# Kernel optimization log

Hardware: AMD Instinct MI355X
Metric: run time of the kernel (lower is better)

The kernel has to match this reference:

```python
import jax, jax.numpy as jnp
import numpy as np

BATCH, SEQ, D_IN, D_OUT = 32, 1024, 128, 128
NEG_SLOPE = 0.1


def setup_inputs() -> dict:
    key = jax.random.key(0)
    k1, k2, k3, k4 = jax.random.split(key, 4)
    nodes = jax.random.normal(k1, (BATCH, SEQ, D_IN), dtype=jnp.float32)
    adjacent = jax.random.randint(k2, (BATCH, SEQ, SEQ), 0, 2, dtype=jnp.int32)
    W = jax.random.normal(k3, (D_IN, D_OUT), dtype=jnp.float32) / np.sqrt(D_IN)
    B = jax.random.normal(k4, (D_IN, D_OUT), dtype=jnp.float32) / np.sqrt(D_IN)
    return {"nodes": nodes, "adjacent": adjacent, "W": W, "B": B}


def reference(nodes, adjacent, W, B):
    # mask[b, out, in] = 1 if edge (out -> in) present
    mask = (adjacent != 0).astype(nodes.dtype)
    # counts[b, in] = in-degree (number of 'out' neighbors pooled per target node)
    counts = mask.sum(axis=1)                               # [b, s_in]
    # segment-sum of neighbor features: pooled[b, in, d] = sum_out mask * nodes[b, out, d]
    pooled = jnp.einsum('boi,bod->bid', mask, nodes)        # [b, s_in, d]
    # mean over neighbors; nodes with zero degree get no pooled contribution
    pooled = jnp.where(counts[..., None] > 0,
                       pooled / jnp.maximum(counts, 1.0)[..., None],
                       jnp.zeros((), dtype=nodes.dtype))
    updated = nodes @ B + pooled @ W                        # [b, s, d_out]
    return jax.nn.leaky_relu(updated, negative_slope=NEG_SLOPE)
```

## Files before the change

kernel.cpp:

```cpp
#include <hip/hip_runtime.h>
#include <hip/hip_bf16.h>

#define SEQ 1024
#define DIM 128
#define NEG_SLOPE 0.1f

typedef __bf16 bf16x8 __attribute__((ext_vector_type(8)));
typedef float f32x4v __attribute__((ext_vector_type(4)));
typedef unsigned short ushort8 __attribute__((ext_vector_type(8)));

__global__ __launch_bounds__(256, 2)
void gcn_fused(const float* __restrict__ nodes,
               const int* __restrict__ adj,
               const float* __restrict__ W,
               const float* __restrict__ Bm,
               float* __restrict__ out)
{
    __shared__ float inv_lds[64];
    __shared__ __bf16 pooled_lds[64][136];

    const int bid   = blockIdx.x;
    const int xcd   = bid & 7;
    const int slot  = bid >> 3;
    const int batch = ((slot >> 4) << 3) | xcd;
    const int mtile = slot & 15;
    const int i0    = mtile << 6;

    const int tid  = threadIdx.x;
    const int wave = tid >> 6;
    const int lane = tid & 63;
    const int wm   = wave >> 1;
    const int wn   = wave & 1;
    const int lrow = lane & 15;
    const int quad = lane >> 4;

    const int*   __restrict__ adj_b   = adj   + (size_t)batch * SEQ * SEQ;
    const float* __restrict__ nodes_b = nodes + (size_t)batch * SEQ * DIM;

    f32x4v acc[2][4] = {};
    int cnt0 = 0, cnt1 = 0;

    const int i_a0 = i0 + wm * 32 + lrow;
    const int d_b0 = wn * 64 + lrow;

    const int*   pa = adj_b   + (size_t)(quad * 8) * SEQ + i_a0;
    const float* pb = nodes_b + (size_t)(quad * 8) * DIM + d_b0;

    #pragma unroll 2
    for (int ks = 0; ks < 32; ++ks) {
        ushort8 au0, au1;
        bf16x8  bv[4];
        #pragma unroll
        for (int j = 0; j < 8; ++j) {
            const int x0 = pa[(size_t)j * SEQ];
            const int x1 = pa[(size_t)j * SEQ + 16];
            cnt0 += (x0 != 0);
            cnt1 += (x1 != 0);
            au0[j] = (x0 != 0) ? (unsigned short)0x3F80 : (unsigned short)0;
            au1[j] = (x1 != 0) ? (unsigned short)0x3F80 : (unsigned short)0;
        }
        #pragma unroll
        for (int nf = 0; nf < 4; ++nf) {
            #pragma unroll
            for (int j = 0; j < 8; ++j)
                bv[nf][j] = (__bf16)pb[j * DIM + nf * 16];
        }
        const bf16x8 av0 = __builtin_bit_cast(bf16x8, au0);
        const bf16x8 av1 = __builtin_bit_cast(bf16x8, au1);
        #pragma unroll
        for (int nf = 0; nf < 4; ++nf)
            acc[0][nf] = __builtin_amdgcn_mfma_f32_16x16x32_bf16(av0, bv[nf], acc[0][nf], 0, 0, 0);
        #pragma unroll
        for (int nf = 0; nf < 4; ++nf)
            acc[1][nf] = __builtin_amdgcn_mfma_f32_16x16x32_bf16(av1, bv[nf], acc[1][nf], 0, 0, 0);
        pa += 32 * SEQ;
        pb += 32 * DIM;
    }

    {
        int c0 = cnt0;
        c0 += __shfl_xor(c0, 16);
        c0 += __shfl_xor(c0, 32);
        int c1 = cnt1;
        c1 += __shfl_xor(c1, 16);
        c1 += __shfl_xor(c1, 32);
        if (wn == 0 && quad == 0) {
            inv_lds[wm * 32 + lrow]      = (c0 > 0) ? 1.0f / (float)c0 : 0.0f;
            inv_lds[wm * 32 + 16 + lrow] = (c1 > 0) ? 1.0f / (float)c1 : 0.0f;
        }
    }
    __syncthreads();

    #pragma unroll
    for (int mf = 0; mf < 2; ++mf) {
        #pragma unroll
        for (int r = 0; r < 4; ++r) {
            const int row = wm * 32 + mf * 16 + quad * 4 + r;
            const float inv = inv_lds[row];
            #pragma unroll
            for (int nf = 0; nf < 4; ++nf) {
                const int col = wn * 64 + nf * 16 + lrow;
                pooled_lds[row][col] = (__bf16)(acc[mf][nf][r] * inv);
            }
        }
    }
    __syncthreads();

    f32x4v acc2[2][4] = {};

    #pragma unroll
    for (int ks = 0; ks < 4; ++ks) {
        const int k0 = ks * 32 + quad * 8;
        bf16x8 av[2];
        #pragma unroll
        for (int mf = 0; mf < 2; ++mf)
            av[mf] = *(const bf16x8*)&pooled_lds[wm * 32 + mf * 16 + lrow][k0];
        bf16x8 bv[4];
        const float* pw = W + (size_t)k0 * DIM + d_b0;
        #pragma unroll
        for (int nf = 0; nf < 4; ++nf) {
            #pragma unroll
            for (int j = 0; j < 8; ++j)
                bv[nf][j] = (__bf16)pw[j * DIM + nf * 16];
        }
        #pragma unroll
        for (int mf = 0; mf < 2; ++mf) {
            #pragma unroll
            for (int nf = 0; nf < 4; ++nf)
                acc2[mf][nf] = __builtin_amdgcn_mfma_f32_16x16x32_bf16(av[mf], bv[nf], acc2[mf][nf], 0, 0, 0);
        }
    }

    #pragma unroll
    for (int ks = 0; ks < 4; ++ks) {
        const int k0 = ks * 32 + quad * 8;
        bf16x8 av[2];
        #pragma unroll
        for (int mf = 0; mf < 2; ++mf) {
            const float* p = nodes_b + (size_t)(i0 + wm * 32 + mf * 16 + lrow) * DIM + k0;
            const float4 f1 = *(const float4*)p;
            const float4 f2 = *(const float4*)(p + 4);
            av[mf][0] = (__bf16)f1.x; av[mf][1] = (__bf16)f1.y;
            av[mf][2] = (__bf16)f1.z; av[mf][3] = (__bf16)f1.w;
            av[mf][4] = (__bf16)f2.x; av[mf][5] = (__bf16)f2.y;
            av[mf][6] = (__bf16)f2.z; av[mf][7] = (__bf16)f2.w;
        }
        bf16x8 bv[4];
        const float* pB = Bm + (size_t)k0 * DIM + d_b0;
        #pragma unroll
        for (int nf = 0; nf < 4; ++nf) {
            #pragma unroll
            for (int j = 0; j < 8; ++j)
                bv[nf][j] = (__bf16)pB[j * DIM + nf * 16];
        }
        #pragma unroll
        for (int mf = 0; mf < 2; ++mf) {
            #pragma unroll
            for (int nf = 0; nf < 4; ++nf)
                acc2[mf][nf] = __builtin_amdgcn_mfma_f32_16x16x32_bf16(av[mf], bv[nf], acc2[mf][nf], 0, 0, 0);
        }
    }

    float* out_b = out + (size_t)batch * SEQ * DIM;
    #pragma unroll
    for (int mf = 0; mf < 2; ++mf) {
        #pragma unroll
        for (int nf = 0; nf < 4; ++nf) {
            const int col = wn * 64 + nf * 16 + lrow;
            #pragma unroll
            for (int r = 0; r < 4; ++r) {
                const int row = i0 + wm * 32 + mf * 16 + quad * 4 + r;
                const float x = acc2[mf][nf][r];
                out_b[(size_t)row * DIM + col] = (x > 0.0f) ? x : NEG_SLOPE * x;
            }
        }
    }
}

extern "C" void kernel_launch(void* const* d_in, const int* in_sizes, int n_in,
                              void* d_out, int out_size, void* d_ws, size_t ws_size,
                              hipStream_t stream) {
    const float* nodes = (const float*)d_in[0];
    const int*   adj   = (const int*)d_in[1];
    const float* W     = (const float*)d_in[2];
    const float* Bm    = (const float*)d_in[3];
    float*       out   = (float*)d_out;
    gcn_fused<<<dim3(512), dim3(256), 0, stream>>>(nodes, adj, W, Bm, out);
}
```

Baseline: 257.0 us.

## Stage adjacency and node tiles through LDS with vectorized loads and register prefetch

The main aggregation loop now loads 64-row chunks of adjacency and node features with 128-bit global loads into registers. It converts them to bf16, writes them transposed into LDS, and reads MFMA fragments from LDS, replacing the earlier scattered scalar global loads. The next chunk is prefetched into registers while the current chunk is computed. In-degree counts now come from an extra MFMA against a ones vector instead of scalar counters and shuffles. This adds two barriers per chunk and more LDS traffic, and uses a union to reuse the LDS space for the pooled tile.

```diff
diff --git a/kernel.cpp b/kernel.cpp
--- a/kernel.cpp
+++ b/kernel.cpp
@@ -7,7 +7,24 @@
 
 typedef __bf16 bf16x8 __attribute__((ext_vector_type(8)));
 typedef float f32x4v __attribute__((ext_vector_type(4)));
-typedef unsigned short ushort8 __attribute__((ext_vector_type(8)));
+
+union LdsU {
+    struct {
+        unsigned short mask_t[64][72];
+        unsigned short nodes_t[128][72];
+    } s;
+    unsigned short pooled[64][136];
+};
+
+__device__ __forceinline__ unsigned short bfb(float f) {
+    __bf16 h = (__bf16)f;
+    return __builtin_bit_cast(unsigned short, h);
+}
+__device__ __forceinline__ unsigned mpack(int x0, int x1) {
+    unsigned m0 = (x0 != 0) ? 0x3F80u : 0u;
+    unsigned m1 = (x1 != 0) ? 0x3F80u : 0u;
+    return m0 | (m1 << 16);
+}
 
 __global__ __launch_bounds__(256, 2)
 void gcn_fused(const float* __restrict__ nodes,
@@ -16,8 +33,7 @@
                const float* __restrict__ Bm,
                float* __restrict__ out)
 {
-    __shared__ float inv_lds[64];
-    __shared__ __bf16 pooled_lds[64][136];
+    __shared__ LdsU u;
 
     const int bid   = blockIdx.x;
     const int xcd   = bid & 7;
@@ -37,76 +53,96 @@
     const int*   __restrict__ adj_b   = adj   + (size_t)batch * SEQ * SEQ;
     const float* __restrict__ nodes_b = nodes + (size_t)batch * SEQ * DIM;
 
+    const int a_row = (tid >> 4) * 4;
+    const int a_col = (tid & 15) * 4;
+    const int n_row = (tid >> 5) * 4;
+    const int n_col = (tid & 31) * 4;
+
     f32x4v acc[2][4] = {};
-    int cnt0 = 0, cnt1 = 0;
-
-    const int i_a0 = i0 + wm * 32 + lrow;
-    const int d_b0 = wn * 64 + lrow;
-
-    const int*   pa = adj_b   + (size_t)(quad * 8) * SEQ + i_a0;
-    const float* pb = nodes_b + (size_t)(quad * 8) * DIM + d_b0;
-
-    #pragma unroll 2
-    for (int ks = 0; ks < 32; ++ks) {
-        ushort8 au0, au1;
-        bf16x8  bv[4];
-        #pragma unroll
-        for (int j = 0; j < 8; ++j) {
-            const int x0 = pa[(size_t)j * SEQ];
-            const int x1 = pa[(size_t)j * SEQ + 16];
-            cnt0 += (x0 != 0);
-            cnt1 += (x1 != 0);
-            au0[j] = (x0 != 0) ? (unsigned short)0x3F80 : (unsigned short)0;
-            au1[j] = (x1 != 0) ? (unsigned short)0x3F80 : (unsigned short)0;
-        }
-        #pragma unroll
-        for (int nf = 0; nf < 4; ++nf) {
-            #pragma unroll
-            for (int j = 0; j < 8; ++j)
-                bv[nf][j] = (__bf16)pb[j * DIM + nf * 16];
-        }
-        const bf16x8 av0 = __builtin_bit_cast(bf16x8, au0);
-        const bf16x8 av1 = __builtin_bit_cast(bf16x8, au1);
-        #pragma unroll
-        for (int nf = 0; nf < 4; ++nf)
-            acc[0][nf] = __builtin_amdgcn_mfma_f32_16x16x32_bf16(av0, bv[nf], acc[0][nf], 0, 0, 0);
-        #pragma unroll
-        for (int nf = 0; nf < 4; ++nf)
-            acc[1][nf] = __builtin_amdgcn_mfma_f32_16x16x32_bf16(av1, bv[nf], acc[1][nf], 0, 0, 0);
-        pa += 32 * SEQ;
-        pb += 32 * DIM;
-    }
-
-    {
-        int c0 = cnt0;
-        c0 += __shfl_xor(c0, 16);
-        c0 += __shfl_xor(c0, 32);
-        int c1 = cnt1;
-        c1 += __shfl_xor(c1, 16);
-        c1 += __shfl_xor(c1, 32);
-        if (wn == 0 && quad == 0) {
-            inv_lds[wm * 32 + lrow]      = (c0 > 0) ? 1.0f / (float)c0 : 0.0f;
-            inv_lds[wm * 32 + 16 + lrow] = (c1 > 0) ? 1.0f / (float)c1 : 0.0f;
-        }
-    }
+    f32x4v acc_cnt[2] = {};
+
+    bf16x8 ones;
+    #pragma unroll
+    for (int j = 0; j < 8; ++j) ones[j] = __builtin_bit_cast(__bf16, (unsigned short)0x3F80);
+
+    int4   A[4];
+    float4 N[8];
+
+    auto load_chunk = [&](int o0) {
+        const int* pa = adj_b + (size_t)(o0 + a_row) * SEQ + (i0 + a_col);
+        #pragma unroll
+        for (int r = 0; r < 4; ++r) A[r] = *(const int4*)(pa + (size_t)r * SEQ);
+        const float* pn = nodes_b + (size_t)(o0 + n_row) * DIM + n_col;
+        #pragma unroll
+        for (int it = 0; it < 2; ++it)
+            #pragma unroll
+            for (int r = 0; r < 4; ++r)
+                N[it * 4 + r] = *(const float4*)(pn + (size_t)(it * 32 + r) * DIM);
+    };
+
+    load_chunk(0);
+
+    for (int chunk = 0; chunk < 16; ++chunk) {
+        __syncthreads();
+        #pragma unroll
+        for (int j = 0; j < 4; ++j) {
+            uint2 w;
+            w.x = mpack(((const int*)&A[0])[j], ((const int*)&A[1])[j]);
+            w.y = mpack(((const int*)&A[2])[j], ((const int*)&A[3])[j]);
+            *(uint2*)&u.s.mask_t[a_col + j][a_row] = w;
+        }
+        #pragma unroll
+        for (int it = 0; it < 2; ++it) {
+            #pragma unroll
+            for (int j = 0; j < 4; ++j) {
+                uint2 w;
+                w.x = (unsigned)bfb(((const float*)&N[it*4+0])[j]) |
+                      ((unsigned)bfb(((const float*)&N[it*4+1])[j]) << 16);
+                w.y = (unsigned)bfb(((const float*)&N[it*4+2])[j]) |
+                      ((unsigned)bfb(((const float*)&N[it*4+3])[j]) << 16);
+                *(uint2*)&u.s.nodes_t[n_col + j][it * 32 + n_row] = w;
+            }
+        }
+        __syncthreads();
+        if (chunk < 15) load_chunk((chunk + 1) * 64);
+
+        #pragma unroll
+        for (int kk = 0; kk < 2; ++kk) {
+            bf16x8 av[2], bv[4];
+            av[0] = *(const bf16x8*)&u.s.mask_t[wm * 32 + lrow][kk * 32 + quad * 8];
+            av[1] = *(const bf16x8*)&u.s.mask_t[wm * 32 + 16 + lrow][kk * 32 + quad * 8];
+            #pragma unroll
+            for (int nf = 0; nf < 4; ++nf)
+                bv[nf] = *(const bf16x8*)&u.s.nodes_t[wn * 64 + nf * 16 + lrow][kk * 32 + quad * 8];
+            #pragma unroll
+            for (int mf = 0; mf < 2; ++mf) {
+                #pragma unroll
+                for (int nf = 0; nf < 4; ++nf)
+                    acc[mf][nf] = __builtin_amdgcn_mfma_f32_16x16x32_bf16(av[mf], bv[nf], acc[mf][nf], 0, 0, 0);
+                acc_cnt[mf] = __builtin_amdgcn_mfma_f32_16x16x32_bf16(av[mf], ones, acc_cnt[mf], 0, 0, 0);
+            }
+        }
+    }
+
     __syncthreads();
-
     #pragma unroll
     for (int mf = 0; mf < 2; ++mf) {
         #pragma unroll
         for (int r = 0; r < 4; ++r) {
             const int row = wm * 32 + mf * 16 + quad * 4 + r;
-            const float inv = inv_lds[row];
+            const float cnt = acc_cnt[mf][r];
+            const float inv = (cnt > 0.5f) ? 1.0f / cnt : 0.0f;
             #pragma unroll
             for (int nf = 0; nf < 4; ++nf) {
                 const int col = wn * 64 + nf * 16 + lrow;
-                pooled_lds[row][col] = (__bf16)(acc[mf][nf][r] * inv);
+                u.pooled[row][col] = bfb(acc[mf][nf][r] * inv);
             }
         }
     }
     __syncthreads();
 
     f32x4v acc2[2][4] = {};
+    const int d_b0 = wn * 64 + lrow;
 
     #pragma unroll
     for (int ks = 0; ks < 4; ++ks) {
@@ -114,7 +150,7 @@
         bf16x8 av[2];
         #pragma unroll
         for (int mf = 0; mf < 2; ++mf)
-            av[mf] = *(const bf16x8*)&pooled_lds[wm * 32 + mf * 16 + lrow][k0];
+            av[mf] = *(const bf16x8*)&u.pooled[wm * 32 + mf * 16 + lrow][k0];
         bf16x8 bv[4];
         const float* pw = W + (size_t)k0 * DIM + d_b0;
         #pragma unroll
@@ -124,11 +160,10 @@
                 bv[nf][j] = (__bf16)pw[j * DIM + nf * 16];
         }
         #pragma unroll
-        for (int mf = 0; mf < 2; ++mf) {
+        for (int mf = 0; mf < 2; ++mf)
             #pragma unroll
             for (int nf = 0; nf < 4; ++nf)
                 acc2[mf][nf] = __builtin_amdgcn_mfma_f32_16x16x32_bf16(av[mf], bv[nf], acc2[mf][nf], 0, 0, 0);
-        }
     }
 
     #pragma unroll
@@ -154,11 +189,10 @@
                 bv[nf][j] = (__bf16)pB[j * DIM + nf * 16];
         }
         #pragma unroll
-        for (int mf = 0; mf < 2; ++mf) {
+        for (int mf = 0; mf < 2; ++mf)
             #pragma unroll
             for (int nf = 0; nf < 4; ++nf)
                 acc2[mf][nf] = __builtin_amdgcn_mfma_f32_16x16x32_bf16(av[mf], bv[nf], acc2[mf][nf], 0, 0, 0);
-        }
     }
 
     float* out_b = out + (size_t)batch * SEQ * DIM;
```

New measurement: 224.2 us. 1.15x faster.
